# Performance work log

Hardware: AMD Instinct MI355X
Metric: run time of the kernel (lower is better)

The kernel has to match this reference:

```python
import jax, jax.numpy as jnp
import numpy as np
import math

B, N, H, D = 2, 2048, 16, 64
NUM_BUCKETS, MAX_DIST = 32, 128
MODEL = H * D


def _rel_pos_bucket(rel, num_buckets, max_distance):
    # T5-style bucketing (bidirectional): half the buckets for sign, half log-spaced.
    nb = num_buckets // 2
    ret = (rel >= 0).astype(jnp.int32) * nb
    n = jnp.abs(rel)
    max_exact = nb // 2
    is_small = n < max_exact
    n_safe = jnp.maximum(n, 1).astype(jnp.float32)
    val_large = max_exact + (
        jnp.log(n_safe / max_exact) / math.log(max_distance / max_exact) * (nb - max_exact)
    ).astype(jnp.int32)
    val_large = jnp.minimum(val_large, nb - 1)
    return ret + jnp.where(is_small, n, val_large)


def _rel_pos_bias(rel_emb, n, m):
    q_pos = jnp.arange(m - n, m)
    k_pos = jnp.arange(m)
    rel = k_pos[None, :] - q_pos[:, None]            # [n, m]
    buckets = _rel_pos_bucket(rel, NUM_BUCKETS, MAX_DIST)
    bias = rel_emb[buckets]                          # [n, m, h]
    return bias.transpose(2, 0, 1)[None]             # [1, h, n, m]


def setup_inputs() -> dict:
    key = jax.random.key(0)
    ks = jax.random.split(key, 6)
    return {
        "q": jax.random.normal(ks[0], (B, N, MODEL), dtype=jnp.float32),
        "k": jax.random.normal(ks[1], (B, N, MODEL), dtype=jnp.float32),
        "v": jax.random.normal(ks[2], (B, N, MODEL), dtype=jnp.float32),
        "rel_emb": jax.random.normal(ks[3], (NUM_BUCKETS, H), dtype=jnp.float32) * 0.05,
        "w_out": jax.random.normal(ks[4], (MODEL, MODEL), dtype=jnp.float32) * (MODEL ** -0.5),
        "b_out": jax.random.normal(ks[5], (MODEL,), dtype=jnp.float32) * 0.02,
    }


def reference(q, k, v, rel_emb, w_out, b_out):
    b, n, _ = q.shape
    split = lambda x: x.reshape(b, n, H, D).transpose(0, 2, 1, 3)  # b h n d
    qh, kh, vh = split(q), split(k), split(v)
    sim = jnp.einsum('bhnd,bhmd->bhnm', qh, kh)
    sim = (sim + _rel_pos_bias(rel_emb, n, n)) * (D ** -0.5)  # note: scale AFTER bias, as in source
    attn = jax.nn.softmax(sim, axis=-1)
    out = jnp.einsum('bhnm,bhmd->bhnd', attn, vh)
    out = out.transpose(0, 2, 1, 3).reshape(b, n, H * D)
    return out @ w_out.T + b_out
```

## Files before the change

### kernel.cpp

```cpp
#include <hip/hip_runtime.h>

#define BB 2
#define NN 2048
#define HH 16
#define MODEL 1024
#define CSC 0.18033688011112042f

typedef short bf16x8 __attribute__((ext_vector_type(8)));
typedef float f32x4 __attribute__((ext_vector_type(4)));

__device__ __forceinline__ unsigned short f2bf(float x) {
  unsigned int u = __builtin_bit_cast(unsigned int, x);
  u += 0x7fffu + ((u >> 16) & 1u);
  return (unsigned short)(u >> 16);
}

__device__ __forceinline__ unsigned int pack_bf2(float a, float b) {
  unsigned int ua = __builtin_bit_cast(unsigned int, a) + 0x8000u;
  unsigned int ub = __builtin_bit_cast(unsigned int, b) + 0x8000u;
  return __builtin_amdgcn_perm(ub, ua, 0x07060302u);
}

__device__ __forceinline__ float fast_exp2(float x) {
#if __has_builtin(__builtin_amdgcn_exp2f)
  return __builtin_amdgcn_exp2f(x);
#else
  return exp2f(x);
#endif
}

__device__ __forceinline__ f32x4 mfma16(bf16x8 a, bf16x8 b, f32x4 c) {
  return __builtin_amdgcn_mfma_f32_16x16x32_bf16(a, b, c, 0, 0, 0);
}

__device__ __forceinline__ void async_copy16(void* lds_base, const void* g) {
  __builtin_amdgcn_global_load_lds(
      (const __attribute__((address_space(1))) void*)g,
      (__attribute__((address_space(3))) void*)lds_base, 16, 0, 0);
}

__global__ void prep_kernel(const float* __restrict__ q, const float* __restrict__ k,
                            const float* __restrict__ w, const float* __restrict__ v,
                            const float* __restrict__ rel_emb,
                            unsigned short* __restrict__ qb, unsigned short* __restrict__ kb,
                            unsigned short* __restrict__ wb, unsigned short* __restrict__ vt,
                            float* __restrict__ biasTab) {
  __shared__ unsigned short tile[64][65];
  const int NQ4 = BB * NN * MODEL / 4;
  const int blk = blockIdx.x;
  if (blk < 9216) {
    int i = blk * 256 + threadIdx.x;
    const float* src;
    unsigned short* dst;
    int j = i;
    if (i < NQ4) {
      src = q; dst = qb;
    } else if (i < 2 * NQ4) {
      src = k; dst = kb; j = i - NQ4;
    } else {
      src = w; dst = wb; j = i - 2 * NQ4;
    }
    float4 f = reinterpret_cast<const float4*>(src)[j];
    ushort4 u;
    u.x = f2bf(f.x); u.y = f2bf(f.y); u.z = f2bf(f.z); u.w = f2bf(f.w);
    reinterpret_cast<ushort4*>(dst)[j] = u;
  } else if (blk < 10240) {
    const int blk2 = blk - 9216;
    const int n0 = (blk2 & 31) * 64;
    const int bh = blk2 >> 5;
    const int b = bh >> 4, h = bh & 15;
    const int c = threadIdx.x & 63;
    const int r = threadIdx.x >> 6;
#pragma unroll
    for (int i = 0; i < 16; ++i) {
      int nl = r * 16 + i;
      tile[c][nl] = f2bf(v[((long)(b * NN + n0 + nl)) * MODEL + h * 64 + c]);
    }
    __syncthreads();
#pragma unroll
    for (int i = 0; i < 16; ++i) {
      int d = r * 16 + i;
      vt[((long)(bh * 64 + d)) * NN + n0 + c] = tile[d][c];
    }
  } else {
    int idx = (blk - 10240) * 256 + threadIdx.x;
    if (idx >= 4095) return;
    int rel = idx - 2047;
    int nn = rel < 0 ? -rel : rel;
    int bucket;
    if (nn < 8) {
      bucket = nn;
    } else {
      float val = logf((float)nn * 0.125f) / logf(16.0f) * 8.0f;
      int vl = 8 + (int)val;
      if (vl > 15) vl = 15;
      bucket = vl;
    }
    if (rel >= 0) bucket += 16;
#pragma unroll
    for (int h = 0; h < 16; ++h)
      biasTab[h * 4095 + idx] = rel_emb[bucket * 16 + h] * CSC - 12.0f;
  }
}

__global__ __launch_bounds__(256, 2) void flash7(
    const unsigned short* __restrict__ qb, const unsigned short* __restrict__ kb,
    const unsigned short* __restrict__ vtb, const float* __restrict__ biasTab,
    unsigned short* __restrict__ attn) {
  __shared__ __align__(16) float obuf[4 * 64 * 68];
  __shared__ __align__(16) float scratch[512];

  const int i = blockIdx.x;
  const int bh = (i & 7) * 4 + ((i >> 3) >> 5);
  const int qt = (i >> 3) & 31;
  const int b = bh >> 4, h = bh & 15;
  const int q0 = qt * 64;
  const int tid = threadIdx.x, w = tid >> 6, lane = tid & 63;
  const int g = lane >> 4, c = lane & 15;

  const float* btab = biasTab + h * 4095 + 2047;
  for (int j = tid; j < 441; j += 256) scratch[j] = btab[j - 220];
  const float cPos = btab[200], cNeg = btab[-200];
  __syncthreads();

  bf16x8 qf0[4], qf1[4];
  const unsigned short* qbase = qb + ((long)(b * NN + q0)) * MODEL + h * 64;
#pragma unroll
  for (int nt = 0; nt < 4; ++nt) {
    const unsigned short* r = qbase + (16 * nt + c) * MODEL + 8 * g;
    qf0[nt] = *reinterpret_cast<const bf16x8*>(r);
    qf1[nt] = *reinterpret_cast<const bf16x8*>(r + 32);
  }

  const unsigned short* kbase = kb + ((long)b * NN) * MODEL + h * 64;
  const unsigned short* vbase = vtb + ((long)bh * 64) * NN;

  f32x4 o[4][4];
  float l_p[4] = {0.f, 0.f, 0.f, 0.f};
#pragma unroll
  for (int mt = 0; mt < 4; ++mt)
#pragma unroll
    for (int nt = 0; nt < 4; ++nt) o[mt][nt] = f32x4{0.f, 0.f, 0.f, 0.f};

  unsigned int* Pb = reinterpret_cast<unsigned int*>(obuf);

  for (int it = 0; it < 8; ++it) {
    const int kt = w + 4 * it;
    bf16x8 kf0[4], kf1[4];
    const unsigned short* krow = kbase + (long)(kt * 64) * MODEL;
#pragma unroll
    for (int mt = 0; mt < 4; ++mt) {
      const unsigned short* r = krow + (16 * mt + c) * MODEL + 8 * g;
      kf0[mt] = *reinterpret_cast<const bf16x8*>(r);
      kf1[mt] = *reinterpret_cast<const bf16x8*>(r + 32);
    }
    bf16x8 vf0[4], vf1[4];
    const unsigned short* vrow = vbase + kt * 64;
#pragma unroll
    for (int mt = 0; mt < 4; ++mt) {
      const unsigned short* r = vrow + (long)(16 * mt + c) * NN + 8 * g;
      vf0[mt] = *reinterpret_cast<const bf16x8*>(r);
      vf1[mt] = *reinterpret_cast<const bf16x8*>(r + 32);
    }
    const int lo = kt * 64 - q0 - 63, hi = kt * 64 + 63 - q0;
    const bool sat = (lo >= 91 || hi <= -91);
    const float cb = (lo >= 91) ? cPos : cNeg;

#pragma unroll
    for (int nt = 0; nt < 4; ++nt) {
      f32x4 s[4];
#pragma unroll
      for (int mt = 0; mt < 4; ++mt) {
        s[mt] = mfma16(kf0[mt], qf0[nt], f32x4{0.f, 0.f, 0.f, 0.f});
        s[mt] = mfma16(kf1[mt], qf1[nt], s[mt]);
      }
      if (sat) {
#pragma unroll
        for (int mt = 0; mt < 4; ++mt)
#pragma unroll
          for (int rr = 0; rr < 4; ++rr) s[mt][rr] = s[mt][rr] * CSC + cb;
      } else {
        const int base = kt * 64 + 4 * g - q0 - 16 * nt - c + 220;
#pragma unroll
        for (int mt = 0; mt < 4; ++mt)
#pragma unroll
          for (int rr = 0; rr < 4; ++rr)
            s[mt][rr] = s[mt][rr] * CSC + scratch[base + 16 * mt + rr];
      }
      float sum = 0.f;
      unsigned int pk[4][2];
#pragma unroll
      for (int mt = 0; mt < 4; ++mt) {
        const float p0 = fast_exp2(s[mt][0]);
        const float p1 = fast_exp2(s[mt][1]);
        const float p2 = fast_exp2(s[mt][2]);
        const float p3 = fast_exp2(s[mt][3]);
        sum += (p0 + p1) + (p2 + p3);
        pk[mt][0] = pack_bf2(p0, p1);
        pk[mt][1] = pack_bf2(p2, p3);
      }
      l_p[nt] += sum;
      const int preg = (w * 4 + nt) * 576 + c * 36;
#pragma unroll
      for (int mt = 0; mt < 4; ++mt)
        *reinterpret_cast<uint2*>(&Pb[preg + 2 * g + 8 * mt]) =
            uint2{pk[mt][0], pk[mt][1]};
      const bf16x8 pb0 = *reinterpret_cast<const bf16x8*>(&Pb[preg + 4 * g]);
      const bf16x8 pb1 = *reinterpret_cast<const bf16x8*>(&Pb[preg + 4 * g + 16]);
#pragma unroll
      for (int mt = 0; mt < 4; ++mt) {
        o[mt][nt] = mfma16(vf0[mt], pb0, o[mt][nt]);
        o[mt][nt] = mfma16(vf1[mt], pb1, o[mt][nt]);
      }
    }
  }

  __syncthreads();
  float* ob = obuf + w * 64 * 68;
#pragma unroll
  for (int nt = 0; nt < 4; ++nt) {
    ob[(16 * nt + c) * 68 + 64 + g] = l_p[nt];
#pragma unroll
    for (int mt = 0; mt < 4; ++mt)
      *reinterpret_cast<f32x4*>(&ob[(16 * nt + c) * 68 + 16 * mt + 4 * g]) = o[mt][nt];
  }
  __syncthreads();

  const int qr = 16 * w + c;
  float l = 0.f;
#pragma unroll
  for (int u = 0; u < 4; ++u)
#pragma unroll
    for (int gg = 0; gg < 4; ++gg) l += obuf[(u * 64 + qr) * 68 + 64 + gg];
  const float inv = 1.f / l;

  float acc[16];
#pragma unroll
  for (int j = 0; j < 16; ++j) acc[j] = 0.f;
#pragma unroll
  for (int u = 0; u < 4; ++u) {
    const float* src = obuf + (u * 64 + qr) * 68;
    f32x4 r0 = *reinterpret_cast<const f32x4*>(&src[8 * g]);
    f32x4 r1 = *reinterpret_cast<const f32x4*>(&src[8 * g + 4]);
    f32x4 r2 = *reinterpret_cast<const f32x4*>(&src[32 + 8 * g]);
    f32x4 r3 = *reinterpret_cast<const f32x4*>(&src[32 + 8 * g + 4]);
#pragma unroll
    for (int j = 0; j < 4; ++j) {
      acc[j] += r0[j];
      acc[4 + j] += r1[j];
      acc[8 + j] += r2[j];
      acc[12 + j] += r3[j];
    }
  }
  unsigned int od[8];
#pragma unroll
  for (int t = 0; t < 8; ++t) od[t] = pack_bf2(acc[2 * t] * inv, acc[2 * t + 1] * inv);
  unsigned short* orow = attn + ((long)(b * NN + q0 + qr)) * MODEL + h * 64;
  *reinterpret_cast<uint4*>(orow + 8 * g) = uint4{od[0], od[1], od[2], od[3]};
  *reinterpret_cast<uint4*>(orow + 32 + 8 * g) = uint4{od[4], od[5], od[6], od[7]};
}

__global__ void proj_gemm_kernel(const unsigned short* __restrict__ A,
                                 const unsigned short* __restrict__ Bw,
                                 const float* __restrict__ bias,
                                 float* __restrict__ out) {
  __shared__ __align__(16) unsigned short At[128 * 64];
  __shared__ __align__(16) unsigned short Bt[64 * 64];
  int bm0 = blockIdx.x * 128, bn0 = blockIdx.y * 64;
  int tid = threadIdx.x, w = tid >> 6, lane = tid & 63;
  int g = lane >> 4, c = lane & 15;
  int m0 = (w & 1) * 64, n0 = (w >> 1) * 32;

  f32x4 acc[4][2];
#pragma unroll
  for (int mi = 0; mi < 4; ++mi)
#pragma unroll
    for (int nj = 0; nj < 2; ++nj) acc[mi][nj] = f32x4{0.f, 0.f, 0.f, 0.f};

  int rloc = lane >> 3, p = lane & 7;
  for (int kt = 0; kt < 16; ++kt) {
    __syncthreads();
#pragma unroll
    for (int t = 0; t < 4; ++t) {
      int row = w * 32 + t * 8 + rloc;
      async_copy16(&At[(w * 32 + t * 8) * 64],
                   A + (long)(bm0 + row) * 1024 + kt * 64 + (p ^ rloc) * 8);
    }
#pragma unroll
    for (int t = 0; t < 2; ++t) {
      int row = w * 16 + t * 8 + rloc;
      async_copy16(&Bt[(w * 16 + t * 8) * 64],
                   Bw + (long)(bn0 + row) * 1024 + kt * 64 + (p ^ rloc) * 8);
    }
    __syncthreads();

    bf16x8 af0[4], af1[4], bf0[2], bf1[2];
#pragma unroll
    for (int mi = 0; mi < 4; ++mi) {
      int row = m0 + 16 * mi + c, sw = row & 7;
      af0[mi] = *reinterpret_cast<const bf16x8*>(&At[row * 64 + (g ^ sw) * 8]);
      af1[mi] = *reinterpret_cast<const bf16x8*>(&At[row * 64 + ((4 + g) ^ sw) * 8]);
    }
#pragma unroll
    for (int nj = 0; nj < 2; ++nj) {
      int row = n0 + 16 * nj + c, sw = row & 7;
      bf0[nj] = *reinterpret_cast<const bf16x8*>(&Bt[row * 64 + (g ^ sw) * 8]);
      bf1[nj] = *reinterpret_cast<const bf16x8*>(&Bt[row * 64 + ((4 + g) ^ sw) * 8]);
    }
#pragma unroll
    for (int mi = 0; mi < 4; ++mi)
#pragma unroll
      for (int nj = 0; nj < 2; ++nj) {
        acc[mi][nj] = mfma16(af0[mi], bf0[nj], acc[mi][nj]);
        acc[mi][nj] = mfma16(af1[mi], bf1[nj], acc[mi][nj]);
      }
  }

#pragma unroll
  for (int mi = 0; mi < 4; ++mi)
#pragma unroll
    for (int nj = 0; nj < 2; ++nj)
#pragma unroll
      for (int r = 0; r < 4; ++r) {
        int row = bm0 + m0 + mi * 16 + 4 * g + r;
        int col = bn0 + n0 + nj * 16 + c;
        out[(long)row * 1024 + col] = acc[mi][nj][r] + bias[col];
      }
}

extern "C" void kernel_launch(void* const* d_in, const int* in_sizes, int n_in,
                              void* d_out, int out_size, void* d_ws, size_t ws_size,
                              hipStream_t stream) {
  const float* q = (const float*)d_in[0];
  const float* k = (const float*)d_in[1];
  const float* v = (const float*)d_in[2];
  const float* rel_emb = (const float*)d_in[3];
  const float* w_out = (const float*)d_in[4];
  const float* b_out = (const float*)d_in[5];
  float* out = (float*)d_out;

  char* ws = (char*)d_ws;
  unsigned short* qb   = (unsigned short*)(ws);
  unsigned short* kb   = (unsigned short*)(ws + (8u << 20));
  unsigned short* vt   = (unsigned short*)(ws + (16u << 20));
  unsigned short* attn = (unsigned short*)(ws + (24u << 20));
  unsigned short* wb   = (unsigned short*)(ws + (32u << 20));
  float* biasTab       = (float*)(ws + (34u << 20));

  hipLaunchKernelGGL(prep_kernel, dim3(10257), dim3(256), 0, stream,
                     q, k, w_out, v, rel_emb, qb, kb, wb, vt, biasTab);
  hipLaunchKernelGGL(flash7, dim3(1024), dim3(256), 0, stream,
                     qb, kb, vt, biasTab, attn);
  hipLaunchKernelGGL(proj_gemm_kernel, dim3(32, 16), dim3(256), 0, stream,
                     attn, wb, b_out, out);
}
```

Before: 189.0 us.

## Raise flash kernel occupancy by reusing K/V registers and halving reduction LDS

The attention kernel now targets three blocks per CU instead of two. To fit, the K and V fragments share one register array: all four score tiles are computed and written to LDS first, then V is loaded into the same registers for the P·V MFMAs. The cross-wave reduction is restructured into two steps, with waves 2-3 adding into waves 0-1. This shrinks the output LDS buffer to about 36KB. The split of the nt loop adds an extra LDS round trip pass, puts the V load later on the critical path, and adds more barriers to the epilogue. The tighter register cap may also cause spilling.

```diff
diff --git a/kernel.cpp b/kernel.cpp
--- a/kernel.cpp
+++ b/kernel.cpp
@@ -103,11 +103,11 @@
   }
 }
 
-__global__ __launch_bounds__(256, 2) void flash7(
+__global__ __launch_bounds__(256, 3) void flash8(
     const unsigned short* __restrict__ qb, const unsigned short* __restrict__ kb,
     const unsigned short* __restrict__ vtb, const float* __restrict__ biasTab,
     unsigned short* __restrict__ attn) {
-  __shared__ __align__(16) float obuf[4 * 64 * 68];
+  __shared__ __align__(16) float obuf[9216];
   __shared__ __align__(16) float scratch[512];
 
   const int i = blockIdx.x;
@@ -146,21 +146,13 @@
 
   for (int it = 0; it < 8; ++it) {
     const int kt = w + 4 * it;
-    bf16x8 kf0[4], kf1[4];
+    bf16x8 kv0[4], kv1[4];
     const unsigned short* krow = kbase + (long)(kt * 64) * MODEL;
 #pragma unroll
     for (int mt = 0; mt < 4; ++mt) {
       const unsigned short* r = krow + (16 * mt + c) * MODEL + 8 * g;
-      kf0[mt] = *reinterpret_cast<const bf16x8*>(r);
-      kf1[mt] = *reinterpret_cast<const bf16x8*>(r + 32);
-    }
-    bf16x8 vf0[4], vf1[4];
-    const unsigned short* vrow = vbase + kt * 64;
-#pragma unroll
-    for (int mt = 0; mt < 4; ++mt) {
-      const unsigned short* r = vrow + (long)(16 * mt + c) * NN + 8 * g;
-      vf0[mt] = *reinterpret_cast<const bf16x8*>(r);
-      vf1[mt] = *reinterpret_cast<const bf16x8*>(r + 32);
+      kv0[mt] = *reinterpret_cast<const bf16x8*>(r);
+      kv1[mt] = *reinterpret_cast<const bf16x8*>(r + 32);
     }
     const int lo = kt * 64 - q0 - 63, hi = kt * 64 + 63 - q0;
     const bool sat = (lo >= 91 || hi <= -91);
@@ -171,8 +163,8 @@
       f32x4 s[4];
 #pragma unroll
       for (int mt = 0; mt < 4; ++mt) {
-        s[mt] = mfma16(kf0[mt], qf0[nt], f32x4{0.f, 0.f, 0.f, 0.f});
-        s[mt] = mfma16(kf1[mt], qf1[nt], s[mt]);
+        s[mt] = mfma16(kv0[mt], qf0[nt], f32x4{0.f, 0.f, 0.f, 0.f});
+        s[mt] = mfma16(kv1[mt], qf1[nt], s[mt]);
       }
       if (sat) {
 #pragma unroll
@@ -205,41 +197,80 @@
       for (int mt = 0; mt < 4; ++mt)
         *reinterpret_cast<uint2*>(&Pb[preg + 2 * g + 8 * mt]) =
             uint2{pk[mt][0], pk[mt][1]};
+    }
+
+    const unsigned short* vrow = vbase + kt * 64;
+#pragma unroll
+    for (int mt = 0; mt < 4; ++mt) {
+      const unsigned short* r = vrow + (long)(16 * mt + c) * NN + 8 * g;
+      kv0[mt] = *reinterpret_cast<const bf16x8*>(r);
+      kv1[mt] = *reinterpret_cast<const bf16x8*>(r + 32);
+    }
+
+#pragma unroll
+    for (int nt = 0; nt < 4; ++nt) {
+      const int preg = (w * 4 + nt) * 576 + c * 36;
       const bf16x8 pb0 = *reinterpret_cast<const bf16x8*>(&Pb[preg + 4 * g]);
       const bf16x8 pb1 = *reinterpret_cast<const bf16x8*>(&Pb[preg + 4 * g + 16]);
 #pragma unroll
       for (int mt = 0; mt < 4; ++mt) {
-        o[mt][nt] = mfma16(vf0[mt], pb0, o[mt][nt]);
-        o[mt][nt] = mfma16(vf1[mt], pb1, o[mt][nt]);
-      }
-    }
-  }
-
-  __syncthreads();
-  float* ob = obuf + w * 64 * 68;
-#pragma unroll
-  for (int nt = 0; nt < 4; ++nt) {
-    ob[(16 * nt + c) * 68 + 64 + g] = l_p[nt];
-#pragma unroll
-    for (int mt = 0; mt < 4; ++mt)
-      *reinterpret_cast<f32x4*>(&ob[(16 * nt + c) * 68 + 16 * mt + 4 * g]) = o[mt][nt];
+        o[mt][nt] = mfma16(kv0[mt], pb0, o[mt][nt]);
+        o[mt][nt] = mfma16(kv1[mt], pb1, o[mt][nt]);
+      }
+    }
+  }
+
+  __syncthreads();
+  if (w >= 2) {
+    float* ob = obuf + (w - 2) * 4352;
+#pragma unroll
+    for (int nt = 0; nt < 4; ++nt) {
+      ob[(16 * nt + c) * 68 + 64 + g] = l_p[nt];
+#pragma unroll
+      for (int mt = 0; mt < 4; ++mt)
+        *reinterpret_cast<f32x4*>(&ob[(16 * nt + c) * 68 + 16 * mt + 4 * g]) = o[mt][nt];
+    }
+  }
+  __syncthreads();
+  if (w < 2) {
+    const float* ob = obuf + w * 4352;
+#pragma unroll
+    for (int nt = 0; nt < 4; ++nt) {
+      l_p[nt] += ob[(16 * nt + c) * 68 + 64 + g];
+#pragma unroll
+      for (int mt = 0; mt < 4; ++mt) {
+        const f32x4 t = *reinterpret_cast<const f32x4*>(&ob[(16 * nt + c) * 68 + 16 * mt + 4 * g]);
+        o[mt][nt] += t;
+      }
+    }
+  }
+  __syncthreads();
+  if (w < 2) {
+    float* ob = obuf + w * 4352;
+#pragma unroll
+    for (int nt = 0; nt < 4; ++nt) {
+      ob[(16 * nt + c) * 68 + 64 + g] = l_p[nt];
+#pragma unroll
+      for (int mt = 0; mt < 4; ++mt)
+        *reinterpret_cast<f32x4*>(&ob[(16 * nt + c) * 68 + 16 * mt + 4 * g]) = o[mt][nt];
+    }
   }
   __syncthreads();
 
   const int qr = 16 * w + c;
   float l = 0.f;
 #pragma unroll
-  for (int u = 0; u < 4; ++u)
-#pragma unroll
-    for (int gg = 0; gg < 4; ++gg) l += obuf[(u * 64 + qr) * 68 + 64 + gg];
+  for (int u = 0; u < 2; ++u)
+#pragma unroll
+    for (int gg = 0; gg < 4; ++gg) l += obuf[u * 4352 + qr * 68 + 64 + gg];
   const float inv = 1.f / l;
 
   float acc[16];
 #pragma unroll
   for (int j = 0; j < 16; ++j) acc[j] = 0.f;
 #pragma unroll
-  for (int u = 0; u < 4; ++u) {
-    const float* src = obuf + (u * 64 + qr) * 68;
+  for (int u = 0; u < 2; ++u) {
+    const float* src = obuf + u * 4352 + qr * 68;
     f32x4 r0 = *reinterpret_cast<const f32x4*>(&src[8 * g]);
     f32x4 r1 = *reinterpret_cast<const f32x4*>(&src[8 * g + 4]);
     f32x4 r2 = *reinterpret_cast<const f32x4*>(&src[32 + 8 * g]);
@@ -349,7 +380,7 @@
 
   hipLaunchKernelGGL(prep_kernel, dim3(10257), dim3(256), 0, stream,
                      q, k, w_out, v, rel_emb, qb, kb, wb, vt, biasTab);
-  hipLaunchKernelGGL(flash7, dim3(1024), dim3(256), 0, stream,
+  hipLaunchKernelGGL(flash8, dim3(1024), dim3(256), 0, stream,
                      qb, kb, vt, biasTab, attn);
   hipLaunchKernelGGL(proj_gemm_kernel, dim3(32, 16), dim3(256), 0, stream,
                      attn, wb, b_out, out);
```

Result: slower. 293.0 us (+55.0%).

## Split flash warps across query and key halves; double-buffer projection GEMM

Applied to the files above, without the earlier changes.

The attention kernel now assigns each warp 32 query rows and half of the key tiles, instead of 64 rows and a quarter of the keys. This cuts per-warp accumulator registers so launch bounds can allow 3 blocks per CU, and the final cross-warp reduction becomes a two-way sum in shared memory. The trade-off is that each K/V tile is now loaded by two warps, which doubles K/V fragment loads. Separately, the output projection GEMM double-buffers its LDS tiles so the async loads for the next k-step overlap the MFMAs on the current one, and one barrier per iteration is removed.

```diff
diff --git a/kernel.cpp b/kernel.cpp
--- a/kernel.cpp
+++ b/kernel.cpp
@@ -103,11 +103,11 @@
   }
 }
 
-__global__ __launch_bounds__(256, 2) void flash7(
+__global__ __launch_bounds__(256, 3) void flash9(
     const unsigned short* __restrict__ qb, const unsigned short* __restrict__ kb,
     const unsigned short* __restrict__ vtb, const float* __restrict__ biasTab,
     unsigned short* __restrict__ attn) {
-  __shared__ __align__(16) float obuf[4 * 64 * 68];
+  __shared__ __align__(16) float obuf[4608];
   __shared__ __align__(16) float scratch[512];
 
   const int i = blockIdx.x;
@@ -117,16 +117,18 @@
   const int q0 = qt * 64;
   const int tid = threadIdx.x, w = tid >> 6, lane = tid & 63;
   const int g = lane >> 4, c = lane & 15;
+  const int wq = w >> 1, wk = w & 1;
+  const int qh0 = q0 + 32 * wq;
 
   const float* btab = biasTab + h * 4095 + 2047;
   for (int j = tid; j < 441; j += 256) scratch[j] = btab[j - 220];
   const float cPos = btab[200], cNeg = btab[-200];
   __syncthreads();
 
-  bf16x8 qf0[4], qf1[4];
-  const unsigned short* qbase = qb + ((long)(b * NN + q0)) * MODEL + h * 64;
-#pragma unroll
-  for (int nt = 0; nt < 4; ++nt) {
+  bf16x8 qf0[2], qf1[2];
+  const unsigned short* qbase = qb + ((long)(b * NN + qh0)) * MODEL + h * 64;
+#pragma unroll
+  for (int nt = 0; nt < 2; ++nt) {
     const unsigned short* r = qbase + (16 * nt + c) * MODEL + 8 * g;
     qf0[nt] = *reinterpret_cast<const bf16x8*>(r);
     qf1[nt] = *reinterpret_cast<const bf16x8*>(r + 32);
@@ -135,17 +137,17 @@
   const unsigned short* kbase = kb + ((long)b * NN) * MODEL + h * 64;
   const unsigned short* vbase = vtb + ((long)bh * 64) * NN;
 
-  f32x4 o[4][4];
-  float l_p[4] = {0.f, 0.f, 0.f, 0.f};
+  f32x4 o[4][2];
+  float l_p[2] = {0.f, 0.f};
 #pragma unroll
   for (int mt = 0; mt < 4; ++mt)
 #pragma unroll
-    for (int nt = 0; nt < 4; ++nt) o[mt][nt] = f32x4{0.f, 0.f, 0.f, 0.f};
+    for (int nt = 0; nt < 2; ++nt) o[mt][nt] = f32x4{0.f, 0.f, 0.f, 0.f};
 
   unsigned int* Pb = reinterpret_cast<unsigned int*>(obuf);
 
-  for (int it = 0; it < 8; ++it) {
-    const int kt = w + 4 * it;
+  for (int it = 0; it < 16; ++it) {
+    const int kt = wk + 2 * it;
     bf16x8 kf0[4], kf1[4];
     const unsigned short* krow = kbase + (long)(kt * 64) * MODEL;
 #pragma unroll
@@ -162,12 +164,12 @@
       vf0[mt] = *reinterpret_cast<const bf16x8*>(r);
       vf1[mt] = *reinterpret_cast<const bf16x8*>(r + 32);
     }
-    const int lo = kt * 64 - q0 - 63, hi = kt * 64 + 63 - q0;
+    const int lo = kt * 64 - qh0 - 31, hi = kt * 64 + 63 - qh0;
     const bool sat = (lo >= 91 || hi <= -91);
     const float cb = (lo >= 91) ? cPos : cNeg;
 
 #pragma unroll
-    for (int nt = 0; nt < 4; ++nt) {
+    for (int nt = 0; nt < 2; ++nt) {
       f32x4 s[4];
 #pragma unroll
       for (int mt = 0; mt < 4; ++mt) {
@@ -180,7 +182,7 @@
 #pragma unroll
           for (int rr = 0; rr < 4; ++rr) s[mt][rr] = s[mt][rr] * CSC + cb;
       } else {
-        const int base = kt * 64 + 4 * g - q0 - 16 * nt - c + 220;
+        const int base = kt * 64 + 4 * g - qh0 - 16 * nt - c + 220;
 #pragma unroll
         for (int mt = 0; mt < 4; ++mt)
 #pragma unroll
@@ -200,7 +202,7 @@
         pk[mt][1] = pack_bf2(p2, p3);
       }
       l_p[nt] += sum;
-      const int preg = (w * 4 + nt) * 576 + c * 36;
+      const int preg = (w * 2 + nt) * 576 + c * 36;
 #pragma unroll
       for (int mt = 0; mt < 4; ++mt)
         *reinterpret_cast<uint2*>(&Pb[preg + 2 * g + 8 * mt]) =
@@ -216,45 +218,49 @@
   }
 
   __syncthreads();
-  float* ob = obuf + w * 64 * 68;
-#pragma unroll
-  for (int nt = 0; nt < 4; ++nt) {
-    ob[(16 * nt + c) * 68 + 64 + g] = l_p[nt];
-#pragma unroll
-    for (int mt = 0; mt < 4; ++mt)
-      *reinterpret_cast<f32x4*>(&ob[(16 * nt + c) * 68 + 16 * mt + 4 * g]) = o[mt][nt];
+  if (wk == 1) {
+    float* ob = obuf + wq * 2176;
+#pragma unroll
+    for (int nt = 0; nt < 2; ++nt) {
+      ob[(16 * nt + c) * 68 + 64 + g] = l_p[nt];
+#pragma unroll
+      for (int mt = 0; mt < 4; ++mt)
+        *reinterpret_cast<f32x4*>(&ob[(16 * nt + c) * 68 + 16 * mt + 4 * g]) = o[mt][nt];
+    }
   }
   __syncthreads();
+  if (wk == 0) {
+    float* ob = obuf + wq * 2176;
+#pragma unroll
+    for (int nt = 0; nt < 2; ++nt) {
+      ob[(16 * nt + c) * 68 + 64 + g] += l_p[nt];
+#pragma unroll
+      for (int mt = 0; mt < 4; ++mt) {
+        f32x4* p = reinterpret_cast<f32x4*>(&ob[(16 * nt + c) * 68 + 16 * mt + 4 * g]);
+        *p += o[mt][nt];
+      }
+    }
+  }
+  __syncthreads();
 
   const int qr = 16 * w + c;
-  float l = 0.f;
-#pragma unroll
-  for (int u = 0; u < 4; ++u)
-#pragma unroll
-    for (int gg = 0; gg < 4; ++gg) l += obuf[(u * 64 + qr) * 68 + 64 + gg];
+  const float* src = obuf + (w >> 1) * 2176 + (16 * (w & 1) + c) * 68;
+  const float l = (src[64] + src[65]) + (src[66] + src[67]);
   const float inv = 1.f / l;
 
-  float acc[16];
-#pragma unroll
-  for (int j = 0; j < 16; ++j) acc[j] = 0.f;
-#pragma unroll
-  for (int u = 0; u < 4; ++u) {
-    const float* src = obuf + (u * 64 + qr) * 68;
-    f32x4 r0 = *reinterpret_cast<const f32x4*>(&src[8 * g]);
-    f32x4 r1 = *reinterpret_cast<const f32x4*>(&src[8 * g + 4]);
-    f32x4 r2 = *reinterpret_cast<const f32x4*>(&src[32 + 8 * g]);
-    f32x4 r3 = *reinterpret_cast<const f32x4*>(&src[32 + 8 * g + 4]);
-#pragma unroll
-    for (int j = 0; j < 4; ++j) {
-      acc[j] += r0[j];
-      acc[4 + j] += r1[j];
-      acc[8 + j] += r2[j];
-      acc[12 + j] += r3[j];
-    }
-  }
+  f32x4 r0 = *reinterpret_cast<const f32x4*>(&src[8 * g]);
+  f32x4 r1 = *reinterpret_cast<const f32x4*>(&src[8 * g + 4]);
+  f32x4 r2 = *reinterpret_cast<const f32x4*>(&src[32 + 8 * g]);
+  f32x4 r3 = *reinterpret_cast<const f32x4*>(&src[32 + 8 * g + 4]);
   unsigned int od[8];
-#pragma unroll
-  for (int t = 0; t < 8; ++t) od[t] = pack_bf2(acc[2 * t] * inv, acc[2 * t + 1] * inv);
+  od[0] = pack_bf2(r0[0] * inv, r0[1] * inv);
+  od[1] = pack_bf2(r0[2] * inv, r0[3] * inv);
+  od[2] = pack_bf2(r1[0] * inv, r1[1] * inv);
+  od[3] = pack_bf2(r1[2] * inv, r1[3] * inv);
+  od[4] = pack_bf2(r2[0] * inv, r2[1] * inv);
+  od[5] = pack_bf2(r2[2] * inv, r2[3] * inv);
+  od[6] = pack_bf2(r3[0] * inv, r3[1] * inv);
+  od[7] = pack_bf2(r3[2] * inv, r3[3] * inv);
   unsigned short* orow = attn + ((long)(b * NN + q0 + qr)) * MODEL + h * 64;
   *reinterpret_cast<uint4*>(orow + 8 * g) = uint4{od[0], od[1], od[2], od[3]};
   *reinterpret_cast<uint4*>(orow + 32 + 8 * g) = uint4{od[4], od[5], od[6], od[7]};
@@ -264,8 +270,8 @@
                                  const unsigned short* __restrict__ Bw,
                                  const float* __restrict__ bias,
                                  float* __restrict__ out) {
-  __shared__ __align__(16) unsigned short At[128 * 64];
-  __shared__ __align__(16) unsigned short Bt[64 * 64];
+  __shared__ __align__(16) unsigned short At[2][128 * 64];
+  __shared__ __align__(16) unsigned short Bt[2][64 * 64];
   int bm0 = blockIdx.x * 128, bn0 = blockIdx.y * 64;
   int tid = threadIdx.x, w = tid >> 6, lane = tid & 63;
   int g = lane >> 4, c = lane & 15;
@@ -278,34 +284,40 @@
     for (int nj = 0; nj < 2; ++nj) acc[mi][nj] = f32x4{0.f, 0.f, 0.f, 0.f};
 
   int rloc = lane >> 3, p = lane & 7;
+
+  auto stage = [&](int buf, int kt) {
+#pragma unroll
+    for (int t = 0; t < 4; ++t) {
+      int row = w * 32 + t * 8 + rloc;
+      async_copy16(&At[buf][(w * 32 + t * 8) * 64],
+                   A + (long)(bm0 + row) * 1024 + kt * 64 + (p ^ rloc) * 8);
+    }
+#pragma unroll
+    for (int t = 0; t < 2; ++t) {
+      int row = w * 16 + t * 8 + rloc;
+      async_copy16(&Bt[buf][(w * 16 + t * 8) * 64],
+                   Bw + (long)(bn0 + row) * 1024 + kt * 64 + (p ^ rloc) * 8);
+    }
+  };
+
+  int cur = 0;
+  stage(0, 0);
   for (int kt = 0; kt < 16; ++kt) {
     __syncthreads();
-#pragma unroll
-    for (int t = 0; t < 4; ++t) {
-      int row = w * 32 + t * 8 + rloc;
-      async_copy16(&At[(w * 32 + t * 8) * 64],
-                   A + (long)(bm0 + row) * 1024 + kt * 64 + (p ^ rloc) * 8);
-    }
-#pragma unroll
-    for (int t = 0; t < 2; ++t) {
-      int row = w * 16 + t * 8 + rloc;
-      async_copy16(&Bt[(w * 16 + t * 8) * 64],
-                   Bw + (long)(bn0 + row) * 1024 + kt * 64 + (p ^ rloc) * 8);
-    }
-    __syncthreads();
+    if (kt < 15) stage(cur ^ 1, kt + 1);
 
     bf16x8 af0[4], af1[4], bf0[2], bf1[2];
 #pragma unroll
     for (int mi = 0; mi < 4; ++mi) {
       int row = m0 + 16 * mi + c, sw = row & 7;
-      af0[mi] = *reinterpret_cast<const bf16x8*>(&At[row * 64 + (g ^ sw) * 8]);
-      af1[mi] = *reinterpret_cast<const bf16x8*>(&At[row * 64 + ((4 + g) ^ sw) * 8]);
+      af0[mi] = *reinterpret_cast<const bf16x8*>(&At[cur][row * 64 + (g ^ sw) * 8]);
+      af1[mi] = *reinterpret_cast<const bf16x8*>(&At[cur][row * 64 + ((4 + g) ^ sw) * 8]);
     }
 #pragma unroll
     for (int nj = 0; nj < 2; ++nj) {
       int row = n0 + 16 * nj + c, sw = row & 7;
-      bf0[nj] = *reinterpret_cast<const bf16x8*>(&Bt[row * 64 + (g ^ sw) * 8]);
-      bf1[nj] = *reinterpret_cast<const bf16x8*>(&Bt[row * 64 + ((4 + g) ^ sw) * 8]);
+      bf0[nj] = *reinterpret_cast<const bf16x8*>(&Bt[cur][row * 64 + (g ^ sw) * 8]);
+      bf1[nj] = *reinterpret_cast<const bf16x8*>(&Bt[cur][row * 64 + ((4 + g) ^ sw) * 8]);
     }
 #pragma unroll
     for (int mi = 0; mi < 4; ++mi)
@@ -314,6 +326,7 @@
         acc[mi][nj] = mfma16(af0[mi], bf0[nj], acc[mi][nj]);
         acc[mi][nj] = mfma16(af1[mi], bf1[nj], acc[mi][nj]);
       }
+    cur ^= 1;
   }
 
 #pragma unroll
@@ -349,7 +362,7 @@
 
   hipLaunchKernelGGL(prep_kernel, dim3(10257), dim3(256), 0, stream,
                      q, k, w_out, v, rel_emb, qb, kb, wb, vt, biasTab);
-  hipLaunchKernelGGL(flash7, dim3(1024), dim3(256), 0, stream,
+  hipLaunchKernelGGL(flash9, dim3(1024), dim3(256), 0, stream,
                      qb, kb, vt, biasTab, attn);
   hipLaunchKernelGGL(proj_gemm_kernel, dim3(32, 16), dim3(256), 0, stream,
                      attn, wb, b_out, out);
```

Result: slower. 239.8 us (+26.9%).
